# Kernel tuning notes

Hardware: AMD Instinct MI355X
Metric: run time of the kernel (lower is better)

Reference implementation:

```python
import jax, jax.numpy as jnp
import numpy as np

NUM_HEADS = 16
HEAD_CH = 64
D_MODEL = 1024  # == NUM_HEADS*HEAD_CH -> out_mapper is Identity


def setup_inputs() -> dict:
    key = jax.random.key(0)
    k1, k2, k3 = jax.random.split(key, 3)
    tokens = jax.random.normal(k1, (2, 2048, D_MODEL), dtype=jnp.float32)
    w_qkv = jax.random.normal(k2, (D_MODEL, 3 * D_MODEL), dtype=jnp.float32) * (1.0 / np.sqrt(D_MODEL))
    b_qkv = jax.random.normal(k3, (3 * D_MODEL,), dtype=jnp.float32) * 0.02
    return {"tokens": tokens, "w_qkv": w_qkv, "b_qkv": b_qkv}


def reference(tokens, w_qkv, b_qkv):
    b, n, _ = tokens.shape
    qkv = tokens @ w_qkv + b_qkv  # [b, n, 3*inner]
    q, k, v = jnp.split(qkv, 3, axis=-1)

    def heads(x):  # [b, n, h*d] -> [b, h, n, d]
        return x.reshape(b, n, NUM_HEADS, HEAD_CH).transpose(0, 2, 1, 3)

    q, k, v = heads(q), heads(k), heads(v)
    scores = jnp.einsum('bhqd,bhkd->bhqk', q, k) / jnp.sqrt(jnp.float32(HEAD_CH))
    attn = jax.nn.softmax(scores, axis=-1)
    out = jnp.einsum('bhqk,bhkd->bhqd', attn, v)  # [b, h, n, d]
    out = out.transpose(0, 2, 1, 3).reshape(b, n, NUM_HEADS * HEAD_CH)
    return out  # out_mapper is Identity since inner_channels == input_channels
```

## Files before the change

kernel.cpp:

```cpp
#include <hip/hip_runtime.h>
#include <stdint.h>

typedef __attribute__((ext_vector_type(8))) short shortx8;
typedef __attribute__((ext_vector_type(4))) float floatx4;
typedef unsigned short bf16_t;

#define NH 16
#define HD 64
#define SEQ 2048
#define BATCH 2
#define DM 1024
#define DM3 3072

#define GLDS(gp, lp) __builtin_amdgcn_global_load_lds( \
    (const __attribute__((address_space(1))) unsigned int*)(gp), \
    (__attribute__((address_space(3))) unsigned int*)(lp), 16, 0, 0)

__device__ __forceinline__ bf16_t f2bf(float f) {
    unsigned int u = __float_as_uint(f);
    u += 0x7fff + ((u >> 16) & 1);
    return (bf16_t)(u >> 16);
}
__device__ __forceinline__ bf16_t f2bf_fast(float f) {
    return (bf16_t)((__float_as_uint(f) + 0x8000u) >> 16);
}

__global__ __launch_bounds__(256) void conv_tokens(const float* __restrict__ in,
                                                   bf16_t* __restrict__ out) {
    int idx = blockIdx.x * 256 + threadIdx.x;
    float4 a = ((const float4*)in)[idx * 2];
    float4 b = ((const float4*)in)[idx * 2 + 1];
    uint4 o;
    o.x = (unsigned)f2bf(a.x) | ((unsigned)f2bf(a.y) << 16);
    o.y = (unsigned)f2bf(a.z) | ((unsigned)f2bf(a.w) << 16);
    o.z = (unsigned)f2bf(b.x) | ((unsigned)f2bf(b.y) << 16);
    o.w = (unsigned)f2bf(b.z) | ((unsigned)f2bf(b.w) << 16);
    ((uint4*)out)[idx] = o;
}

__global__ __launch_bounds__(256) void conv_w(const float* __restrict__ w,
                                              bf16_t* __restrict__ wt) {
    __shared__ bf16_t t[64 * 65];
    const int n0 = blockIdx.x * 64;
    const int k0 = blockIdx.y * 64;
    const int tid = threadIdx.x;
    for (int i = 0; i < 16; i++) {
        int idx = i * 256 + tid;
        int r = idx >> 6, c = idx & 63;
        t[r * 65 + c] = f2bf(w[(k0 + r) * DM3 + n0 + c]);
    }
    __syncthreads();
    for (int i = 0; i < 16; i++) {
        int idx = i * 256 + tid;
        int r = idx >> 6, c = idx & 63;
        wt[(n0 + r) * DM + k0 + c] = t[c * 65 + r];
    }
}


#define QSCALE 0.18033688011f
__global__ __launch_bounds__(256) void qkv_gemm(const bf16_t* __restrict__ A,
                                                const bf16_t* __restrict__ Bt,
                                                const float* __restrict__ bias,
                                                bf16_t* __restrict__ Qo,
                                                bf16_t* __restrict__ Ko,
                                                bf16_t* __restrict__ Vto) {
    __shared__ __align__(16) bf16_t As[128 * 64];
    __shared__ __align__(16) bf16_t Bs[128 * 64];
    const int m0 = blockIdx.x * 128;
    const int n0 = blockIdx.y * 128;
    const int tid = threadIdx.x;
    const int wave = tid >> 6, lane = tid & 63;
    const int quad = lane >> 4, l16 = lane & 15;
    const int wm = (wave & 1) * 64, wn = (wave >> 1) * 64;
    const int srow = tid >> 3;
    const int swz8 = ((tid & 7) ^ (srow & 7)) * 8;
    const int h3 = l16 & 7;
    floatx4 acc[4][4] = {};

    for (int kt = 0; kt < DM; kt += 64) {
        __syncthreads();
        for (int rr = 0; rr < 4; rr++) {
            GLDS(&A[(m0 + rr * 32 + srow) * DM + kt + swz8], &As[rr * 2048 + tid * 8]);
            GLDS(&Bt[(n0 + rr * 32 + srow) * DM + kt + swz8], &Bs[rr * 2048 + tid * 8]);
        }
        __syncthreads();
        for (int ks = 0; ks < 2; ks++) {
            const int g = ((ks * 4 + quad) ^ h3) * 8;
            shortx8 af[4], bfr[4];
            for (int t = 0; t < 4; t++)
                af[t] = *(const shortx8*)&As[(wm + t * 16 + l16) * 64 + g];
            for (int t = 0; t < 4; t++)
                bfr[t] = *(const shortx8*)&Bs[(wn + t * 16 + l16) * 64 + g];
            for (int i = 0; i < 4; i++)
                for (int j = 0; j < 4; j++)
                    acc[i][j] = __builtin_amdgcn_mfma_f32_16x16x32_bf16(af[i], bfr[j], acc[i][j], 0, 0, 0);
        }
    }
    for (int i = 0; i < 4; i++)
        for (int j = 0; j < 4; j++)
            for (int r = 0; r < 4; r++) {
                int m = m0 + wm + i * 16 + quad * 4 + r;
                int n = n0 + wn + j * 16 + l16;
                float v = acc[i][j][r] + bias[n];
                int part = n >> 10;
                int rr = n & 1023;
                int h = rr >> 6, d = rr & 63;
                int b = m >> 11, pos = m & 2047;
                if (part == 0) {
                    Qo[((b * NH + h) * SEQ + pos) * HD + d] = f2bf(v * QSCALE);
                } else if (part == 1) {
                    Ko[((b * NH + h) * SEQ + pos) * HD + d] = f2bf(v);
                } else {
                    Vto[((b * NH + h) * HD + d) * SEQ + pos] = f2bf(v);
                }
            }
}

__global__ __launch_bounds__(256) void attn(const bf16_t* __restrict__ Q,
                                            const bf16_t* __restrict__ K,
                                            const bf16_t* __restrict__ Vt,
                                            float* __restrict__ out) {
    __shared__ __align__(16) bf16_t Qs[128 * 64];
    __shared__ __align__(16) bf16_t Ks[64 * 64];
    __shared__ __align__(16) bf16_t Vs[64 * 64];
    __shared__ __align__(16) bf16_t Ps[128 * 64];
    const int qt_blk = blockIdx.x;
    const int bh = blockIdx.y;
    const int b = bh >> 4, h = bh & 15;
    const int q0 = qt_blk * 128;
    const bf16_t* Qb = Q + ((size_t)bh * SEQ + q0) * HD;
    const bf16_t* Kb = K + (size_t)bh * SEQ * HD;
    const bf16_t* Vb = Vt + (size_t)bh * HD * SEQ;
    const int tid = threadIdx.x;
    const int wave = tid >> 6, lane = tid & 63;
    const int quad = lane >> 4, l16 = lane & 15;
    const int h3 = l16 & 7;
    const int srow = tid >> 3;
    const int swz8 = ((tid & 7) ^ (srow & 7)) * 8;

    for (int rr = 0; rr < 4; rr++)
        GLDS(&Qb[(rr * 32 + srow) * 64 + swz8], &Qs[rr * 2048 + tid * 8]);
    __syncthreads();

    shortx8 qf[2][2];
    for (int qt = 0; qt < 2; qt++)
        for (int kc = 0; kc < 2; kc++)
            qf[qt][kc] = *(const shortx8*)&Qs[(wave * 32 + qt * 16 + l16) * 64 + ((kc * 4 + quad) ^ h3) * 8];

    float m_i[2] = {-1e30f, -1e30f}, l_i[2] = {0.f, 0.f};
    floatx4 acc_o[4][2] = {};

    for (int k0 = 0; k0 < SEQ; k0 += 64) {
        __syncthreads();
        for (int rr = 0; rr < 2; rr++) {
            GLDS(&Kb[(k0 + rr * 32 + srow) * 64 + swz8], &Ks[rr * 2048 + tid * 8]);
            GLDS(&Vb[(size_t)(rr * 32 + srow) * SEQ + k0 + swz8], &Vs[rr * 2048 + tid * 8]);
        }
        __syncthreads();

        floatx4 s[4][2] = {};
        for (int kc = 0; kc < 2; kc++) {
            const int g = ((kc * 4 + quad) ^ h3) * 8;
            shortx8 kf[4];
            for (int kt = 0; kt < 4; kt++)
                kf[kt] = *(const shortx8*)&Ks[(kt * 16 + l16) * 64 + g];
            for (int kt = 0; kt < 4; kt++)
                for (int qt = 0; qt < 2; qt++)
                    s[kt][qt] = __builtin_amdgcn_mfma_f32_16x16x32_bf16(kf[kt], qf[qt][kc], s[kt][qt], 0, 0, 0);
        }

        float alpha[2];
        for (int qt = 0; qt < 2; qt++) {
            float mx = -1e30f;
            for (int kt = 0; kt < 4; kt++)
                for (int r = 0; r < 4; r++) mx = fmaxf(mx, s[kt][qt][r]);
            mx = fmaxf(mx, __shfl_xor(mx, 16, 64));
            mx = fmaxf(mx, __shfl_xor(mx, 32, 64));
            float mnew = fmaxf(m_i[qt], mx);
            float al = __builtin_amdgcn_exp2f(m_i[qt] - mnew);
            m_i[qt] = mnew;
            alpha[qt] = al;
            float rs = 0.f;
            for (int kt = 0; kt < 4; kt++)
                for (int r = 0; r < 4; r++) {
                    float p = __builtin_amdgcn_exp2f(s[kt][qt][r] - mnew);
                    s[kt][qt][r] = p;
                    rs += p;
                }
            rs += __shfl_xor(rs, 16, 64);
            rs += __shfl_xor(rs, 32, 64);
            l_i[qt] = l_i[qt] * al + rs;
        }

        for (int qt = 0; qt < 2; qt++)
            for (int kt = 0; kt < 4; kt++) {
                ushort4 pk;
                pk.x = f2bf_fast(s[kt][qt][0]);
                pk.y = f2bf_fast(s[kt][qt][1]);
                pk.z = f2bf_fast(s[kt][qt][2]);
                pk.w = f2bf_fast(s[kt][qt][3]);
                *(ushort4*)&Ps[(wave * 32 + qt * 16 + l16) * 64 +
                               ((2 * kt + (quad >> 1)) ^ h3) * 8 + (quad & 1) * 4] = pk;
            }

        for (int dt = 0; dt < 4; dt++)
            for (int qt = 0; qt < 2; qt++)
                for (int r = 0; r < 4; r++) acc_o[dt][qt][r] *= alpha[qt];

        for (int kc = 0; kc < 2; kc++) {
            const int g = ((kc * 4 + quad) ^ h3) * 8;
            shortx8 vf[4], pf[2];
            for (int dt = 0; dt < 4; dt++)
                vf[dt] = *(const shortx8*)&Vs[(dt * 16 + l16) * 64 + g];
            for (int qt = 0; qt < 2; qt++)
                pf[qt] = *(const shortx8*)&Ps[(wave * 32 + qt * 16 + l16) * 64 + g];
            for (int dt = 0; dt < 4; dt++)
                for (int qt = 0; qt < 2; qt++)
                    acc_o[dt][qt] = __builtin_amdgcn_mfma_f32_16x16x32_bf16(vf[dt], pf[qt], acc_o[dt][qt], 0, 0, 0);
        }
    }

    for (int qt = 0; qt < 2; qt++) {
        float inv = 1.0f / l_i[qt];
        int q = q0 + wave * 32 + qt * 16 + l16;
        for (int dt = 0; dt < 4; dt++) {
            float4 o;
            o.x = acc_o[dt][qt][0] * inv;
            o.y = acc_o[dt][qt][1] * inv;
            o.z = acc_o[dt][qt][2] * inv;
            o.w = acc_o[dt][qt][3] * inv;
            *(float4*)&out[(size_t)(b * SEQ + q) * DM + h * HD + dt * 16 + quad * 4] = o;
        }
    }
}

extern "C" void kernel_launch(void* const* d_in, const int* in_sizes, int n_in,
                              void* d_out, int out_size, void* d_ws, size_t ws_size,
                              hipStream_t stream) {
    const float* tokens = (const float*)d_in[0];
    const float* w = (const float*)d_in[1];
    const float* bias = (const float*)d_in[2];
    float* out = (float*)d_out;
    char* ws = (char*)d_ws;

    bf16_t* tok_bf = (bf16_t*)(ws);
    bf16_t* wt_bf  = (bf16_t*)(ws + (size_t)8 * 1024 * 1024);
    bf16_t* Qb     = (bf16_t*)(ws + (size_t)14 * 1024 * 1024);
    bf16_t* Kb     = (bf16_t*)(ws + (size_t)22 * 1024 * 1024);
    bf16_t* Vb     = (bf16_t*)(ws + (size_t)30 * 1024 * 1024);

    conv_tokens<<<2048, 256, 0, stream>>>(tokens, tok_bf);
    conv_w<<<dim3(48, 16), 256, 0, stream>>>(w, wt_bf);
    qkv_gemm<<<dim3(32, 24), 256, 0, stream>>>(tok_bf, wt_bf, bias, Qb, Kb, Vb);
    attn<<<dim3(16, 32), 256, 0, stream>>>(Qb, Kb, Vb, out);
}
```

Measured before the change: 188.7 us.

## Double-buffer K/V in attention, widen per-wave Q tile, stage V-transpose through LDS

The attention kernel drops to 128 threads (2 waves), each handling 64 query rows, and double-buffers the K/V tiles so the next tile's global-to-LDS load overlaps compute, with one barrier per iteration. Softmax probabilities are truncated to bf16 with a byte permute, and the row sum is built from the truncated values. In the QKV GEMM, the V-part epilogue stages bf16 results through LDS so the transposed V stores become coalesced 16-byte writes instead of scattered 2-byte stores. The risks are fewer resident waves per CU from launch_bounds(128,1) and more registers, plus slightly different rounding of P.

```diff
diff --git a/kernel.cpp b/kernel.cpp
--- a/kernel.cpp
+++ b/kernel.cpp
@@ -20,9 +20,6 @@
     unsigned int u = __float_as_uint(f);
     u += 0x7fff + ((u >> 16) & 1);
     return (bf16_t)(u >> 16);
-}
-__device__ __forceinline__ bf16_t f2bf_fast(float f) {
-    return (bf16_t)((__float_as_uint(f) + 0x8000u) >> 16);
 }
 
 __global__ __launch_bounds__(256) void conv_tokens(const float* __restrict__ in,
@@ -65,8 +62,10 @@
                                                 bf16_t* __restrict__ Qo,
                                                 bf16_t* __restrict__ Ko,
                                                 bf16_t* __restrict__ Vto) {
-    __shared__ __align__(16) bf16_t As[128 * 64];
-    __shared__ __align__(16) bf16_t Bs[128 * 64];
+    __shared__ __align__(16) char smem[128 * 136 * 2];
+    bf16_t* As = (bf16_t*)smem;
+    bf16_t* Bs = As + 128 * 64;
+    bf16_t* Cs = (bf16_t*)smem;
     const int m0 = blockIdx.x * 128;
     const int n0 = blockIdx.y * 128;
     const int tid = threadIdx.x;
@@ -97,33 +96,56 @@
                     acc[i][j] = __builtin_amdgcn_mfma_f32_16x16x32_bf16(af[i], bfr[j], acc[i][j], 0, 0, 0);
         }
     }
-    for (int i = 0; i < 4; i++)
-        for (int j = 0; j < 4; j++)
-            for (int r = 0; r < 4; r++) {
-                int m = m0 + wm + i * 16 + quad * 4 + r;
-                int n = n0 + wn + j * 16 + l16;
-                float v = acc[i][j][r] + bias[n];
-                int part = n >> 10;
-                int rr = n & 1023;
-                int h = rr >> 6, d = rr & 63;
-                int b = m >> 11, pos = m & 2047;
-                if (part == 0) {
-                    Qo[((b * NH + h) * SEQ + pos) * HD + d] = f2bf(v * QSCALE);
-                } else if (part == 1) {
-                    Ko[((b * NH + h) * SEQ + pos) * HD + d] = f2bf(v);
-                } else {
-                    Vto[((b * NH + h) * HD + d) * SEQ + pos] = f2bf(v);
+
+    const int part = n0 >> 10;
+    const int b = m0 >> 11, pos0 = m0 & 2047;
+
+    if (part != 2) {
+        for (int i = 0; i < 4; i++)
+            for (int j = 0; j < 4; j++)
+                for (int r = 0; r < 4; r++) {
+                    int m = m0 + wm + i * 16 + quad * 4 + r;
+                    int n = n0 + wn + j * 16 + l16;
+                    float v = acc[i][j][r] + bias[n];
+                    int rr = n & 1023;
+                    int h = rr >> 6, d = rr & 63;
+                    int pos = m & 2047;
+                    if (part == 0)
+                        Qo[((b * NH + h) * SEQ + pos) * HD + d] = f2bf(v * QSCALE);
+                    else
+                        Ko[((b * NH + h) * SEQ + pos) * HD + d] = f2bf(v);
                 }
+    } else {
+        __syncthreads();
+        for (int i = 0; i < 4; i++)
+            for (int j = 0; j < 4; j++) {
+                int nl = wn + j * 16 + l16;
+                int n = n0 + nl;
+                float bv = bias[n];
+                uint2 pk;
+                pk.x = (unsigned)f2bf(acc[i][j][0] + bv) | ((unsigned)f2bf(acc[i][j][1] + bv) << 16);
+                pk.y = (unsigned)f2bf(acc[i][j][2] + bv) | ((unsigned)f2bf(acc[i][j][3] + bv) << 16);
+                *(uint2*)&Cs[nl * 136 + wm + i * 16 + quad * 4] = pk;
             }
-}
-
-__global__ __launch_bounds__(256) void attn(const bf16_t* __restrict__ Q,
-                                            const bf16_t* __restrict__ K,
-                                            const bf16_t* __restrict__ Vt,
-                                            float* __restrict__ out) {
+        __syncthreads();
+        for (int p = 0; p < 8; p++) {
+            int nl = p * 16 + (tid >> 4);
+            int g = tid & 15;
+            uint4 v = *(const uint4*)&Cs[nl * 136 + g * 8];
+            int rr = (n0 + nl) & 1023;
+            int h = rr >> 6, d = rr & 63;
+            *(uint4*)&Vto[(size_t)((b * NH + h) * HD + d) * SEQ + pos0 + g * 8] = v;
+        }
+    }
+}
+
+__global__ __launch_bounds__(128, 1) void attn(const bf16_t* __restrict__ Q,
+                                               const bf16_t* __restrict__ K,
+                                               const bf16_t* __restrict__ Vt,
+                                               float* __restrict__ out) {
     __shared__ __align__(16) bf16_t Qs[128 * 64];
-    __shared__ __align__(16) bf16_t Ks[64 * 64];
-    __shared__ __align__(16) bf16_t Vs[64 * 64];
+    __shared__ __align__(16) bf16_t Ks[2][64 * 64];
+    __shared__ __align__(16) bf16_t Vs[2][64 * 64];
     __shared__ __align__(16) bf16_t Ps[128 * 64];
     const int qt_blk = blockIdx.x;
     const int bh = blockIdx.y;
@@ -139,91 +161,95 @@
     const int srow = tid >> 3;
     const int swz8 = ((tid & 7) ^ (srow & 7)) * 8;
 
-    for (int rr = 0; rr < 4; rr++)
-        GLDS(&Qb[(rr * 32 + srow) * 64 + swz8], &Qs[rr * 2048 + tid * 8]);
+    for (int rr = 0; rr < 8; rr++)
+        GLDS(&Qb[(rr * 16 + srow) * 64 + swz8], &Qs[rr * 1024 + tid * 8]);
+
+    for (int rr = 0; rr < 4; rr++) {
+        GLDS(&Kb[(rr * 16 + srow) * 64 + swz8], &Ks[0][rr * 1024 + tid * 8]);
+        GLDS(&Vb[(size_t)(rr * 16 + srow) * SEQ + swz8], &Vs[0][rr * 1024 + tid * 8]);
+    }
     __syncthreads();
 
-    shortx8 qf[2][2];
-    for (int qt = 0; qt < 2; qt++)
+    shortx8 qf[4][2];
+    for (int qt = 0; qt < 4; qt++)
         for (int kc = 0; kc < 2; kc++)
-            qf[qt][kc] = *(const shortx8*)&Qs[(wave * 32 + qt * 16 + l16) * 64 + ((kc * 4 + quad) ^ h3) * 8];
-
-    float m_i[2] = {-1e30f, -1e30f}, l_i[2] = {0.f, 0.f};
-    floatx4 acc_o[4][2] = {};
-
-    for (int k0 = 0; k0 < SEQ; k0 += 64) {
-        __syncthreads();
-        for (int rr = 0; rr < 2; rr++) {
-            GLDS(&Kb[(k0 + rr * 32 + srow) * 64 + swz8], &Ks[rr * 2048 + tid * 8]);
-            GLDS(&Vb[(size_t)(rr * 32 + srow) * SEQ + k0 + swz8], &Vs[rr * 2048 + tid * 8]);
-        }
-        __syncthreads();
-
-        floatx4 s[4][2] = {};
+            qf[qt][kc] = *(const shortx8*)&Qs[(wave * 64 + qt * 16 + l16) * 64 + ((kc * 4 + quad) ^ h3) * 8];
+
+    float m_i[4] = {-1e30f, -1e30f, -1e30f, -1e30f};
+    float l_i[4] = {0.f, 0.f, 0.f, 0.f};
+    floatx4 acc_o[4][4] = {};
+
+    for (int it = 0; it < SEQ / 64; ++it) {
+        const int cur = it & 1;
+        if (it + 1 < SEQ / 64) {
+            const int nxt = cur ^ 1, kk = (it + 1) * 64;
+            for (int rr = 0; rr < 4; rr++) {
+                GLDS(&Kb[(kk + rr * 16 + srow) * 64 + swz8], &Ks[nxt][rr * 1024 + tid * 8]);
+                GLDS(&Vb[(size_t)(rr * 16 + srow) * SEQ + kk + swz8], &Vs[nxt][rr * 1024 + tid * 8]);
+            }
+        }
+
+        floatx4 s[4][4] = {};
         for (int kc = 0; kc < 2; kc++) {
             const int g = ((kc * 4 + quad) ^ h3) * 8;
             shortx8 kf[4];
             for (int kt = 0; kt < 4; kt++)
-                kf[kt] = *(const shortx8*)&Ks[(kt * 16 + l16) * 64 + g];
+                kf[kt] = *(const shortx8*)&Ks[cur][(kt * 16 + l16) * 64 + g];
             for (int kt = 0; kt < 4; kt++)
-                for (int qt = 0; qt < 2; qt++)
+                for (int qt = 0; qt < 4; qt++)
                     s[kt][qt] = __builtin_amdgcn_mfma_f32_16x16x32_bf16(kf[kt], qf[qt][kc], s[kt][qt], 0, 0, 0);
         }
 
-        float alpha[2];
-        for (int qt = 0; qt < 2; qt++) {
+        float alpha[4];
+        for (int qt = 0; qt < 4; qt++) {
             float mx = -1e30f;
             for (int kt = 0; kt < 4; kt++)
                 for (int r = 0; r < 4; r++) mx = fmaxf(mx, s[kt][qt][r]);
             mx = fmaxf(mx, __shfl_xor(mx, 16, 64));
             mx = fmaxf(mx, __shfl_xor(mx, 32, 64));
             float mnew = fmaxf(m_i[qt], mx);
-            float al = __builtin_amdgcn_exp2f(m_i[qt] - mnew);
+            alpha[qt] = __builtin_amdgcn_exp2f(m_i[qt] - mnew);
             m_i[qt] = mnew;
-            alpha[qt] = al;
             float rs = 0.f;
-            for (int kt = 0; kt < 4; kt++)
+            for (int kt = 0; kt < 4; kt++) {
+                unsigned u[4];
                 for (int r = 0; r < 4; r++) {
                     float p = __builtin_amdgcn_exp2f(s[kt][qt][r] - mnew);
-                    s[kt][qt][r] = p;
-                    rs += p;
+                    u[r] = __float_as_uint(p);
+                    rs += __uint_as_float(u[r] & 0xffff0000u);
                 }
+                uint2 pk;
+                pk.x = __builtin_amdgcn_perm(u[1], u[0], 0x07060302u);
+                pk.y = __builtin_amdgcn_perm(u[3], u[2], 0x07060302u);
+                *(uint2*)&Ps[(wave * 64 + qt * 16 + l16) * 64 +
+                             ((2 * kt + (quad >> 1)) ^ h3) * 8 + (quad & 1) * 4] = pk;
+            }
             rs += __shfl_xor(rs, 16, 64);
             rs += __shfl_xor(rs, 32, 64);
-            l_i[qt] = l_i[qt] * al + rs;
-        }
-
-        for (int qt = 0; qt < 2; qt++)
-            for (int kt = 0; kt < 4; kt++) {
-                ushort4 pk;
-                pk.x = f2bf_fast(s[kt][qt][0]);
-                pk.y = f2bf_fast(s[kt][qt][1]);
-                pk.z = f2bf_fast(s[kt][qt][2]);
-                pk.w = f2bf_fast(s[kt][qt][3]);
-                *(ushort4*)&Ps[(wave * 32 + qt * 16 + l16) * 64 +
-                               ((2 * kt + (quad >> 1)) ^ h3) * 8 + (quad & 1) * 4] = pk;
-            }
+            l_i[qt] = l_i[qt] * alpha[qt] + rs;
+        }
 
         for (int dt = 0; dt < 4; dt++)
-            for (int qt = 0; qt < 2; qt++)
+            for (int qt = 0; qt < 4; qt++)
                 for (int r = 0; r < 4; r++) acc_o[dt][qt][r] *= alpha[qt];
 
         for (int kc = 0; kc < 2; kc++) {
             const int g = ((kc * 4 + quad) ^ h3) * 8;
-            shortx8 vf[4], pf[2];
+            shortx8 vf[4], pf[4];
             for (int dt = 0; dt < 4; dt++)
-                vf[dt] = *(const shortx8*)&Vs[(dt * 16 + l16) * 64 + g];
-            for (int qt = 0; qt < 2; qt++)
-                pf[qt] = *(const shortx8*)&Ps[(wave * 32 + qt * 16 + l16) * 64 + g];
+                vf[dt] = *(const shortx8*)&Vs[cur][(dt * 16 + l16) * 64 + g];
+            for (int qt = 0; qt < 4; qt++)
+                pf[qt] = *(const shortx8*)&Ps[(wave * 64 + qt * 16 + l16) * 64 + g];
             for (int dt = 0; dt < 4; dt++)
-                for (int qt = 0; qt < 2; qt++)
+                for (int qt = 0; qt < 4; qt++)
                     acc_o[dt][qt] = __builtin_amdgcn_mfma_f32_16x16x32_bf16(vf[dt], pf[qt], acc_o[dt][qt], 0, 0, 0);
         }
-    }
-
-    for (int qt = 0; qt < 2; qt++) {
+        __syncthreads();
+    }
+
+    for (int qt = 0; qt < 4; qt++) {
         float inv = 1.0f / l_i[qt];
-        int q = q0 + wave * 32 + qt * 16 + l16;
+        int q = q0 + wave * 64 + qt * 16 + l16;
         for (int dt = 0; dt < 4; dt++) {
             float4 o;
             o.x = acc_o[dt][qt][0] * inv;
@@ -253,5 +279,5 @@
     conv_tokens<<<2048, 256, 0, stream>>>(tokens, tok_bf);
     conv_w<<<dim3(48, 16), 256, 0, stream>>>(w, wt_bf);
     qkv_gemm<<<dim3(32, 24), 256, 0, stream>>>(tok_bf, wt_bf, bias, Qb, Kb, Vb);
-    attn<<<dim3(16, 32), 256, 0, stream>>>(Qb, Kb, Vb, out);
-}
+    attn<<<dim3(16, 32), 128, 0, stream>>>(Qb, Kb, Vb, out);
+}
```

Measured after the change: 208.4 us. 1.1x slower.
